# Performance work log

Measured on AMD Instinct MI355X. Metric: run time of the kernel, lower is better.

## Reference

```python
import jax, jax.numpy as jnp
import numpy as np

BN_EPS = 1e-5

def _batchnorm(x):
    # BatchNorm1d(affine=False) in training mode: per-feature batch stats, biased var
    m = jnp.mean(x, axis=0)
    v = jnp.var(x, axis=0)
    return (x - m) * jax.lax.rsqrt(v + BN_EPS)

def setup_inputs() -> dict:
    key = jax.random.key(0)
    ks = jax.random.split(key, 8)
    B, S, H, I = 2, 2048, 1024, 4096
    NE, NS, K = 16384, 128, 16
    return {
        "hidden_states": jax.random.normal(ks[0], (B, S, H), dtype=jnp.float32),
        "gate_w": jax.random.normal(ks[1], (I, H), dtype=jnp.float32) * 0.02,
        "up_w": jax.random.normal(ks[2], (I, H), dtype=jnp.float32) * 0.02,
        "down_w": jax.random.normal(ks[3], (H, I), dtype=jnp.float32) * 0.02,
        "router_x_w": jax.random.normal(ks[4], (NS, H), dtype=jnp.float32) * 0.02,
        "router_y_w": jax.random.normal(ks[5], (NS, H), dtype=jnp.float32) * 0.02,
        "up_embed": jax.random.normal(ks[6], (NE, H), dtype=jnp.float32) * 0.02,
        "down_embed": jax.random.normal(ks[7], (NE, H), dtype=jnp.float32) * 0.02,
        "top_k": K,
    }

def reference(hidden_states, gate_w, up_w, down_w, router_x_w, router_y_w, up_embed, down_embed, top_k):
    B, S, H = hidden_states.shape
    ns = router_x_w.shape[0]  # num_expert_sqrt
    x = hidden_states.reshape(-1, H)  # [N, H], N = B*S

    # product-key router: two grid log-softmaxes, outer-sum, global top-k
    lpx = jax.nn.log_softmax(_batchnorm(x @ router_x_w.T), axis=-1)  # [N, ns]
    lpy = jax.nn.log_softmax(_batchnorm(x @ router_y_w.T), axis=-1)  # [N, ns]
    all_scores = (lpx[:, :, None] + lpy[:, None, :]).reshape(-1, ns * ns)  # [N, ns^2]
    scores, indices = jax.lax.top_k(all_scores, top_k)  # [N, k]
    routing_weights = jnp.exp(scores)

    # per-token expert embedding gather + small bmm chain (PEER-style)
    ue = up_embed[indices]    # [N, k, H]
    de = down_embed[indices]  # [N, k, H]
    ew = jnp.einsum('nkh,nh->nk', ue, x)
    ew = jax.nn.silu(ew) * routing_weights
    experts_states = jnp.einsum('nk,nkh->nh', ew, de).reshape(B, S, H)

    # dense gated MLP
    dense = (jax.nn.silu(x @ gate_w.T) * (x @ up_w.T)) @ down_w.T
    return dense.reshape(B, S, H) + experts_states
```

## Files before the change

kernel.cpp:

```cpp
#include <hip/hip_runtime.h>

typedef float f32x4 __attribute__((ext_vector_type(4)));
typedef short bf16x8 __attribute__((ext_vector_type(8)));
typedef unsigned short u16;

#define NEG_INF (-1e30f)

__device__ __forceinline__ u16 f2bf(float f) {
    unsigned u = __builtin_bit_cast(unsigned, f);
    unsigned r = u + 0x7FFFu + ((u >> 16) & 1u);
    return (u16)(r >> 16);
}

__device__ __forceinline__ float wave_max(float v) {
    #pragma unroll
    for (int o = 32; o > 0; o >>= 1) v = fmaxf(v, __shfl_xor(v, o, 64));
    return v;
}
__device__ __forceinline__ float wave_sum(float v) {
    #pragma unroll
    for (int o = 32; o > 0; o >>= 1) v += __shfl_xor(v, o, 64);
    return v;
}
__device__ __forceinline__ void wave_argmax(float& v, int& i) {
    #pragma unroll
    for (int o = 32; o > 0; o >>= 1) {
        float ov = __shfl_xor(v, o, 64);
        int oi = __shfl_xor(i, o, 64);
        if (ov > v || (ov == v && oi < i)) { v = ov; i = oi; }
    }
}

__device__ __forceinline__ void g2l16(const void* g, void* l) {
    __builtin_amdgcn_global_load_lds((__attribute__((address_space(1))) void*)g,
                                     (__attribute__((address_space(3))) void*)l,
                                     16, 0, 0);
}

template<int NROUND>
__device__ __forceinline__ void stage_bf16(const u16* __restrict__ src, int ld,
                                           u16* dst, int tid) {
    #pragma unroll
    for (int r = 0; r < NROUND; ++r) {
        int e = r * 2048 + tid * 8;
        int row = e >> 6, col = e & 63;
        g2l16(src + (size_t)row * ld + col, dst + e);
    }
}

__device__ __forceinline__ void stage_f32_128(const float* __restrict__ src, int ld,
                                              u16* dst, int tid) {
    #pragma unroll
    for (int r = 0; r < 4; ++r) {
        int e = r * 2048 + tid * 8;
        int row = e >> 6, col = e & 63;
        const float* s = src + (size_t)row * ld + col;
        float4 a = *reinterpret_cast<const float4*>(s);
        float4 b = *reinterpret_cast<const float4*>(s + 4);
        uint4 pk;
        pk.x = (unsigned)f2bf(a.x) | ((unsigned)f2bf(a.y) << 16);
        pk.y = (unsigned)f2bf(a.z) | ((unsigned)f2bf(a.w) << 16);
        pk.z = (unsigned)f2bf(b.x) | ((unsigned)f2bf(b.y) << 16);
        pk.w = (unsigned)f2bf(b.z) | ((unsigned)f2bf(b.w) << 16);
        *reinterpret_cast<uint4*>(dst + e) = pk;
    }
}

__device__ __forceinline__ bf16x8 frag(const u16* lds, int row0, int ks, int lane) {
    return *reinterpret_cast<const bf16x8*>(
        lds + (row0 + (lane & 15)) * 64 + ks * 32 + (lane >> 4) * 8);
}


template<bool ABF, bool ADD>
__global__ __launch_bounds__(256, 2) void gemm_bt64(
    const float* __restrict__ Af, const u16* __restrict__ Ab, const u16* __restrict__ B,
    float* __restrict__ C, int K, int ldA, int ldB, int ldC) {
    __shared__ u16 As[8192];
    __shared__ u16 Bs[4096];
    int tid = threadIdx.x, lane = tid & 63, wave = tid >> 6;
    int rowBase = blockIdx.y * 128, colBase = blockIdx.x * 64;
    int wm = (wave >> 1) * 64, wn = (wave & 1) * 32;
    f32x4 acc[4][2] = {};
    for (int k0 = 0; k0 < K; k0 += 64) {
        if constexpr (ABF) stage_bf16<4>(Ab + (size_t)rowBase * ldA + k0, ldA, As, tid);
        else               stage_f32_128(Af + (size_t)rowBase * ldA + k0, ldA, As, tid);
        stage_bf16<2>(B + (size_t)colBase * ldB + k0, ldB, Bs, tid);
        __syncthreads();
        #pragma unroll
        for (int ks = 0; ks < 2; ++ks) {
            bf16x8 af[4], bfr[2];
            #pragma unroll
            for (int i = 0; i < 4; ++i) af[i] = frag(As, wm + i * 16, ks, lane);
            #pragma unroll
            for (int j = 0; j < 2; ++j) bfr[j] = frag(Bs, wn + j * 16, ks, lane);
            #pragma unroll
            for (int i = 0; i < 4; ++i)
                #pragma unroll
                for (int j = 0; j < 2; ++j)
                    acc[i][j] = __builtin_amdgcn_mfma_f32_16x16x32_bf16(af[i], bfr[j], acc[i][j], 0, 0, 0);
        }
        __syncthreads();
    }
    int rq = (lane >> 4) * 4, cq = lane & 15;
    #pragma unroll
    for (int i = 0; i < 4; ++i)
        #pragma unroll
        for (int j = 0; j < 2; ++j) {
            int col = colBase + wn + j * 16 + cq;
            #pragma unroll
            for (int r = 0; r < 4; ++r) {
                int row = rowBase + wm + i * 16 + rq + r;
                size_t o = (size_t)row * ldC + col;
                if constexpr (ADD) C[o] = acc[i][j][r] + C[o];
                else               C[o] = acc[i][j][r];
            }
        }
}

template<bool ABF>
__global__ __launch_bounds__(256, 2) void gemm_gateup(
    const float* __restrict__ Af, const u16* __restrict__ Ab,
    const u16* __restrict__ G, const u16* __restrict__ U,
    u16* __restrict__ H2, int ldH) {
    __shared__ u16 As[8192];
    __shared__ u16 Gs[4096];
    __shared__ u16 Us[4096];
    int tid = threadIdx.x, lane = tid & 63, wave = tid >> 6;
    int rowBase = blockIdx.y * 128, colBase = blockIdx.x * 64;
    int wm = (wave >> 1) * 64, wn = (wave & 1) * 32;
    f32x4 ag[4][2] = {}, au[4][2] = {};
    for (int k0 = 0; k0 < 1024; k0 += 64) {
        if constexpr (ABF) stage_bf16<4>(Ab + (size_t)rowBase * 1024 + k0, 1024, As, tid);
        else               stage_f32_128(Af + (size_t)rowBase * 1024 + k0, 1024, As, tid);
        stage_bf16<2>(G + (size_t)colBase * 1024 + k0, 1024, Gs, tid);
        stage_bf16<2>(U + (size_t)colBase * 1024 + k0, 1024, Us, tid);
        __syncthreads();
        #pragma unroll
        for (int ks = 0; ks < 2; ++ks) {
            bf16x8 af[4], gf[2], uf[2];
            #pragma unroll
            for (int i = 0; i < 4; ++i) af[i] = frag(As, wm + i * 16, ks, lane);
            #pragma unroll
            for (int j = 0; j < 2; ++j) { gf[j] = frag(Gs, wn + j * 16, ks, lane);
                                          uf[j] = frag(Us, wn + j * 16, ks, lane); }
            #pragma unroll
            for (int i = 0; i < 4; ++i)
                #pragma unroll
                for (int j = 0; j < 2; ++j) {
                    ag[i][j] = __builtin_amdgcn_mfma_f32_16x16x32_bf16(af[i], gf[j], ag[i][j], 0, 0, 0);
                    au[i][j] = __builtin_amdgcn_mfma_f32_16x16x32_bf16(af[i], uf[j], au[i][j], 0, 0, 0);
                }
        }
        __syncthreads();
    }
    int rq = (lane >> 4) * 4, cq = lane & 15;
    #pragma unroll
    for (int i = 0; i < 4; ++i)
        #pragma unroll
        for (int j = 0; j < 2; ++j) {
            int col = colBase + wn + j * 16 + cq;
            #pragma unroll
            for (int r = 0; r < 4; ++r) {
                int row = rowBase + wm + i * 16 + rq + r;
                float g = ag[i][j][r], u = au[i][j][r];
                float h = (g / (1.f + __expf(-g))) * u;
                H2[(size_t)row * ldH + col] = f2bf(h);
            }
        }
}

__global__ void conv_bf16(const float* __restrict__ s, u16* __restrict__ d,
                          int srcLd, int cl2, int total4) {
    int i = blockIdx.x * 256 + threadIdx.x;
    if (i >= total4) return;
    int r = i >> cl2, c = (i & ((1 << cl2) - 1)) * 4;
    float4 v = *reinterpret_cast<const float4*>(s + (size_t)r * srcLd + c);
    ushort4 pk;
    pk.x = f2bf(v.x); pk.y = f2bf(v.y); pk.z = f2bf(v.z); pk.w = f2bf(v.w);
    *reinterpret_cast<ushort4*>(d + (size_t)i * 4) = pk;
}

__global__ void bn_stats(const float* __restrict__ R, float* __restrict__ stats) {
    int c = threadIdx.x;
    int r0 = blockIdx.x * 64;
    float s = 0.f, s2 = 0.f;
    for (int r = r0; r < r0 + 64; ++r) {
        float v = R[(size_t)r * 256 + c];
        s += v; s2 += v * v;
    }
    atomicAdd(&stats[c], s);
    atomicAdd(&stats[256 + c], s2);
}

__global__ __launch_bounds__(64) void router_topk(
    const float* __restrict__ R, const float* __restrict__ stats,
    int* __restrict__ idx_out, float* __restrict__ wt_out) {
    int n = blockIdx.x, lane = threadIdx.x;
    const float invN = 1.0f / 4096.0f;
    float z[4];
    #pragma unroll
    for (int p = 0; p < 4; ++p) {
        int c = p * 64 + lane;
        float mean = stats[c] * invN;
        float var = fmaxf(stats[256 + c] * invN - mean * mean, 0.f);
        float v = R[(size_t)n * 256 + c];
        z[p] = (v - mean) * rsqrtf(var + 1e-5f);
    }
    float mx = wave_max(fmaxf(z[0], z[1]));
    float sx = __logf(wave_sum(__expf(z[0] - mx) + __expf(z[1] - mx)));
    float lx0 = z[0] - mx - sx, lx1 = z[1] - mx - sx;
    float my = wave_max(fmaxf(z[2], z[3]));
    float sy = __logf(wave_sum(__expf(z[2] - my) + __expf(z[3] - my)));
    float ly0 = z[2] - my - sy, ly1 = z[3] - my - sy;

    __shared__ float tx[16], ty[16];
    __shared__ int txc[16], tyc[16];
    float v0 = lx0, v1 = lx1;
    for (int t = 0; t < 16; ++t) {
        float bv; int bc;
        if (v1 > v0) { bv = v1; bc = lane + 64; } else { bv = v0; bc = lane; }
        wave_argmax(bv, bc);
        if (lane == 0) { tx[t] = bv; txc[t] = bc; }
        if (bc == lane) v0 = NEG_INF;
        else if (bc == lane + 64) v1 = NEG_INF;
    }
    v0 = ly0; v1 = ly1;
    for (int t = 0; t < 16; ++t) {
        float bv; int bc;
        if (v1 > v0) { bv = v1; bc = lane + 64; } else { bv = v0; bc = lane; }
        wave_argmax(bv, bc);
        if (lane == 0) { ty[t] = bv; tyc[t] = bc; }
        if (bc == lane) v0 = NEG_INF;
        else if (bc == lane + 64) v1 = NEG_INF;
    }
    __syncthreads();
    float cv[4]; int ci[4];
    #pragma unroll
    for (int p = 0; p < 4; ++p) {
        int pid = p * 64 + lane;
        cv[p] = tx[pid >> 4] + ty[pid & 15];
        ci[p] = pid;
    }
    for (int t = 0; t < 16; ++t) {
        float bv = cv[0]; int bc = ci[0];
        #pragma unroll
        for (int p = 1; p < 4; ++p)
            if (cv[p] > bv) { bv = cv[p]; bc = ci[p]; }
        wave_argmax(bv, bc);
        if (lane == 0) {
            idx_out[n * 16 + t] = txc[bc >> 4] * 128 + tyc[bc & 15];
            wt_out[n * 16 + t] = __expf(bv);
        }
        #pragma unroll
        for (int p = 0; p < 4; ++p)
            if (ci[p] == bc) cv[p] = NEG_INF;
    }
}

__global__ __launch_bounds__(256) void expert_store(
    const float* __restrict__ X, const float* __restrict__ UE, const float* __restrict__ DE,
    const int* __restrict__ idxs, const float* __restrict__ wts, float* __restrict__ Out) {
    int n = blockIdx.x, tid = threadIdx.x;
    int lane = tid & 63, wave = tid >> 6;
    __shared__ float xs[1024];
    __shared__ float ews[16];
    __shared__ int sidx[16];
    __shared__ float swt[16];
    if (tid < 16) {
        sidx[tid] = min(max(idxs[n * 16 + tid], 0), 16383);
        swt[tid] = wts[n * 16 + tid];
    }
    {
        float4 v = reinterpret_cast<const float4*>(X + (size_t)n * 1024)[tid];
        *reinterpret_cast<float4*>(xs + tid * 4) = v;
    }
    __syncthreads();
    #pragma unroll
    for (int q = 0; q < 4; ++q) {
        int e = wave * 4 + q;
        const float* row = UE + (size_t)sidx[e] * 1024;
        float acc = 0.f;
        #pragma unroll
        for (int c = 0; c < 4; ++c) {
            int h = c * 256 + lane * 4;
            float4 a = *reinterpret_cast<const float4*>(row + h);
            float4 xv = *reinterpret_cast<const float4*>(xs + h);
            acc += a.x * xv.x + a.y * xv.y + a.z * xv.z + a.w * xv.w;
        }
        acc = wave_sum(acc);
        if (lane == 0) {
            float s = acc / (1.f + __expf(-acc));
            ews[e] = s * swt[e];
        }
    }
    __syncthreads();
    float4 a = make_float4(0.f, 0.f, 0.f, 0.f);
    int h = tid * 4;
    #pragma unroll
    for (int e = 0; e < 16; ++e) {
        const float* row = DE + (size_t)sidx[e] * 1024;
        float4 v = *reinterpret_cast<const float4*>(row + h);
        float w = ews[e];
        a.x += w * v.x; a.y += w * v.y;
        a.z += w * v.z; a.w += w * v.w;
    }
    reinterpret_cast<float4*>(Out + (size_t)n * 1024)[tid] = a;
}

extern "C" void kernel_launch(void* const* d_in, const int* in_sizes, int n_in,
                              void* d_out, int out_size, void* d_ws, size_t ws_size,
                              hipStream_t stream) {
    const float* x   = (const float*)d_in[0];
    const float* gw  = (const float*)d_in[1];
    const float* uw  = (const float*)d_in[2];
    const float* dw  = (const float*)d_in[3];
    const float* rxw = (const float*)d_in[4];
    const float* ryw = (const float*)d_in[5];
    const float* ue  = (const float*)d_in[6];
    const float* de  = (const float*)d_in[7];
    float* out = (float*)d_out;

    char* p = (char*)d_ws;
    float* stats = (float*)p; p += 16384;
    int*   idxb  = (int*)p;   p += 262144;
    float* wtb   = (float*)p; p += 262144;
    u16*   W     = (u16*)p;   p += 4194304;
    float* R     = (float*)p;
    u16*   H2    = (u16*)p;

    bool useXb = ws_size >= 38289408ull + 8388608ull;
    u16* xb = (u16*)((char*)d_ws + 38289408ull);

    hipMemsetAsync(stats, 0, 512 * sizeof(float), stream);

    conv_bf16<<<128, 256, 0, stream>>>(rxw, W, 1024, 8, 32768);
    conv_bf16<<<128, 256, 0, stream>>>(ryw, W + 131072, 1024, 8, 32768);
    if (useXb) conv_bf16<<<4096, 256, 0, stream>>>(x, xb, 1024, 8, 1048576);

    if (useXb) gemm_bt64<true , false><<<dim3(4, 32), 256, 0, stream>>>(nullptr, xb, W, R, 1024, 1024, 1024, 256);
    else       gemm_bt64<false, false><<<dim3(4, 32), 256, 0, stream>>>(x, nullptr, W, R, 1024, 1024, 1024, 256);

    bn_stats<<<64, 256, 0, stream>>>(R, stats);
    router_topk<<<4096, 64, 0, stream>>>(R, stats, idxb, wtb);
    expert_store<<<4096, 256, 0, stream>>>(x, ue, de, idxb, wtb, out);

    for (int q = 0; q < 4; ++q) {
        conv_bf16<<<1024, 256, 0, stream>>>(gw + (size_t)q * 1048576, W, 1024, 8, 262144);
        conv_bf16<<<1024, 256, 0, stream>>>(uw + (size_t)q * 1048576, W + 1048576, 1024, 8, 262144);
        if (useXb) gemm_gateup<true ><<<dim3(16, 32), 256, 0, stream>>>(nullptr, xb, W, W + 1048576, H2 + q * 1024, 4096);
        else       gemm_gateup<false><<<dim3(16, 32), 256, 0, stream>>>(x, nullptr, W, W + 1048576, H2 + q * 1024, 4096);
    }
    for (int h = 0; h < 2; ++h) {
        conv_bf16<<<2048, 256, 0, stream>>>(dw + h * 2048, W, 4096, 9, 524288);
        gemm_bt64<true, true><<<dim3(16, 32), 256, 0, stream>>>(nullptr, H2 + h * 2048, W, out, 2048, 4096, 2048, 1024);
    }
}
```

Before: 547.5 us.

## Fuse fp32-to-bf16 conversion into GEMM staging and co-schedule expert with gate/up GEMM

Removes all standalone bf16 conversion passes and weight scratch buffers. GEMMs now load fp32 directly and pack to bf16 with the hardware v_cvt_pk_bf16_f32 instruction while staging LDS. The gate/up GEMM runs in one launch interleaved with the per-token expert gather blocks, and the down projection uses an XCD-aware block swizzle. This cuts launches and global traffic for converted copies, but every block that touches a weight tile re-reads and re-converts fp32 weights, and the expert path now shares a kernel whose register and LDS footprint is sized for the GEMM.

```diff
diff --git a/kernel.cpp b/kernel.cpp
--- a/kernel.cpp
+++ b/kernel.cpp
@@ -11,6 +11,11 @@
     unsigned r = u + 0x7FFFu + ((u >> 16) & 1u);
     return (u16)(r >> 16);
 }
+__device__ __forceinline__ unsigned pk2(float a, float b) {
+    unsigned r;
+    asm("v_cvt_pk_bf16_f32 %0, %1, %2" : "=v"(r) : "v"(a), "v"(b));
+    return r;
+}
 
 __device__ __forceinline__ float wave_max(float v) {
     #pragma unroll
@@ -48,20 +53,19 @@
     }
 }
 
-__device__ __forceinline__ void stage_f32_128(const float* __restrict__ src, int ld,
-                                              u16* dst, int tid) {
-    #pragma unroll
-    for (int r = 0; r < 4; ++r) {
+template<int NROUND>
+__device__ __forceinline__ void stage_f32(const float* __restrict__ src, int ld,
+                                          u16* dst, int tid) {
+    #pragma unroll
+    for (int r = 0; r < NROUND; ++r) {
         int e = r * 2048 + tid * 8;
         int row = e >> 6, col = e & 63;
         const float* s = src + (size_t)row * ld + col;
         float4 a = *reinterpret_cast<const float4*>(s);
         float4 b = *reinterpret_cast<const float4*>(s + 4);
         uint4 pk;
-        pk.x = (unsigned)f2bf(a.x) | ((unsigned)f2bf(a.y) << 16);
-        pk.y = (unsigned)f2bf(a.z) | ((unsigned)f2bf(a.w) << 16);
-        pk.z = (unsigned)f2bf(b.x) | ((unsigned)f2bf(b.y) << 16);
-        pk.w = (unsigned)f2bf(b.z) | ((unsigned)f2bf(b.w) << 16);
+        pk.x = pk2(a.x, a.y); pk.y = pk2(a.z, a.w);
+        pk.z = pk2(b.x, b.y); pk.w = pk2(b.z, b.w);
         *reinterpret_cast<uint4*>(dst + e) = pk;
     }
 }
@@ -71,21 +75,20 @@
         lds + (row0 + (lane & 15)) * 64 + ks * 32 + (lane >> 4) * 8);
 }
 
-
-template<bool ABF, bool ADD>
-__global__ __launch_bounds__(256, 2) void gemm_bt64(
-    const float* __restrict__ Af, const u16* __restrict__ Ab, const u16* __restrict__ B,
-    float* __restrict__ C, int K, int ldA, int ldB, int ldC) {
+__global__ __launch_bounds__(256, 2) void gemm_router(
+    const float* __restrict__ X, const float* __restrict__ RX, const float* __restrict__ RY,
+    float* __restrict__ R) {
     __shared__ u16 As[8192];
     __shared__ u16 Bs[4096];
     int tid = threadIdx.x, lane = tid & 63, wave = tid >> 6;
     int rowBase = blockIdx.y * 128, colBase = blockIdx.x * 64;
+    const float* Bp = (blockIdx.x < 2) ? RX + (size_t)colBase * 1024
+                                       : RY + (size_t)(colBase - 128) * 1024;
     int wm = (wave >> 1) * 64, wn = (wave & 1) * 32;
     f32x4 acc[4][2] = {};
-    for (int k0 = 0; k0 < K; k0 += 64) {
-        if constexpr (ABF) stage_bf16<4>(Ab + (size_t)rowBase * ldA + k0, ldA, As, tid);
-        else               stage_f32_128(Af + (size_t)rowBase * ldA + k0, ldA, As, tid);
-        stage_bf16<2>(B + (size_t)colBase * ldB + k0, ldB, Bs, tid);
+    for (int k0 = 0; k0 < 1024; k0 += 64) {
+        stage_f32<4>(X + (size_t)rowBase * 1024 + k0, 1024, As, tid);
+        stage_f32<2>(Bp + k0, 1024, Bs, tid);
         __syncthreads();
         #pragma unroll
         for (int ks = 0; ks < 2; ++ks) {
@@ -111,74 +114,156 @@
             #pragma unroll
             for (int r = 0; r < 4; ++r) {
                 int row = rowBase + wm + i * 16 + rq + r;
-                size_t o = (size_t)row * ldC + col;
-                if constexpr (ADD) C[o] = acc[i][j][r] + C[o];
-                else               C[o] = acc[i][j][r];
-            }
-        }
-}
-
-template<bool ABF>
-__global__ __launch_bounds__(256, 2) void gemm_gateup(
-    const float* __restrict__ Af, const u16* __restrict__ Ab,
-    const u16* __restrict__ G, const u16* __restrict__ U,
-    u16* __restrict__ H2, int ldH) {
+                R[(size_t)row * 256 + col] = acc[i][j][r];
+            }
+        }
+}
+
+__global__ __launch_bounds__(256, 2) void gateup_expert(
+    const float* __restrict__ X, const float* __restrict__ GW, const float* __restrict__ UW,
+    u16* __restrict__ H2,
+    const float* __restrict__ UE, const float* __restrict__ DE,
+    const int* __restrict__ idxs, const float* __restrict__ wts, float* __restrict__ Out) {
+    __shared__ __align__(16) char smem[32768];
+    int b = blockIdx.x, tid = threadIdx.x;
+    int lane = tid & 63, wave = tid >> 6;
+
+    if (b % 3 == 0) {
+        int g = b / 3;
+        int rowBase = (g >> 6) * 128, colBase = (g & 63) * 64;
+        u16* As = (u16*)smem;
+        u16* Gs = (u16*)(smem + 16384);
+        u16* Us = (u16*)(smem + 24576);
+        int wm = (wave >> 1) * 64, wn = (wave & 1) * 32;
+        f32x4 ag[4][2] = {}, au[4][2] = {};
+        for (int k0 = 0; k0 < 1024; k0 += 64) {
+            stage_f32<4>(X + (size_t)rowBase * 1024 + k0, 1024, As, tid);
+            stage_f32<2>(GW + (size_t)colBase * 1024 + k0, 1024, Gs, tid);
+            stage_f32<2>(UW + (size_t)colBase * 1024 + k0, 1024, Us, tid);
+            __syncthreads();
+            #pragma unroll
+            for (int ks = 0; ks < 2; ++ks) {
+                bf16x8 af[4], gf[2], uf[2];
+                #pragma unroll
+                for (int i = 0; i < 4; ++i) af[i] = frag(As, wm + i * 16, ks, lane);
+                #pragma unroll
+                for (int j = 0; j < 2; ++j) { gf[j] = frag(Gs, wn + j * 16, ks, lane);
+                                              uf[j] = frag(Us, wn + j * 16, ks, lane); }
+                #pragma unroll
+                for (int i = 0; i < 4; ++i)
+                    #pragma unroll
+                    for (int j = 0; j < 2; ++j) {
+                        ag[i][j] = __builtin_amdgcn_mfma_f32_16x16x32_bf16(af[i], gf[j], ag[i][j], 0, 0, 0);
+                        au[i][j] = __builtin_amdgcn_mfma_f32_16x16x32_bf16(af[i], uf[j], au[i][j], 0, 0, 0);
+                    }
+            }
+            __syncthreads();
+        }
+        int rq = (lane >> 4) * 4, cq = lane & 15;
+        #pragma unroll
+        for (int i = 0; i < 4; ++i)
+            #pragma unroll
+            for (int j = 0; j < 2; ++j) {
+                int col = colBase + wn + j * 16 + cq;
+                #pragma unroll
+                for (int r = 0; r < 4; ++r) {
+                    int row = rowBase + wm + i * 16 + rq + r;
+                    float gv = ag[i][j][r], uv = au[i][j][r];
+                    float h = (gv / (1.f + __expf(-gv))) * uv;
+                    H2[(size_t)row * 4096 + col] = f2bf(h);
+                }
+            }
+    } else {
+        int n = b - b / 3 - 1;
+        float* xs  = (float*)smem;
+        float* ews = (float*)(smem + 4096);
+        int*  sidx = (int*)(smem + 4160);
+        float* swt = (float*)(smem + 4224);
+        if (tid < 16) {
+            sidx[tid] = min(max(idxs[n * 16 + tid], 0), 16383);
+            swt[tid] = wts[n * 16 + tid];
+        }
+        {
+            float4 v = reinterpret_cast<const float4*>(X + (size_t)n * 1024)[tid];
+            *reinterpret_cast<float4*>(xs + tid * 4) = v;
+        }
+        __syncthreads();
+        #pragma unroll
+        for (int q = 0; q < 4; ++q) {
+            int e = wave * 4 + q;
+            const float* row = UE + (size_t)sidx[e] * 1024;
+            float acc = 0.f;
+            #pragma unroll
+            for (int c = 0; c < 4; ++c) {
+                int h = c * 256 + lane * 4;
+                float4 a = *reinterpret_cast<const float4*>(row + h);
+                float4 xv = *reinterpret_cast<const float4*>(xs + h);
+                acc += a.x * xv.x + a.y * xv.y + a.z * xv.z + a.w * xv.w;
+            }
+            acc = wave_sum(acc);
+            if (lane == 0) {
+                float s = acc / (1.f + __expf(-acc));
+                ews[e] = s * swt[e];
+            }
+        }
+        __syncthreads();
+        float4 a = make_float4(0.f, 0.f, 0.f, 0.f);
+        int h = tid * 4;
+        #pragma unroll
+        for (int e = 0; e < 16; ++e) {
+            const float* row = DE + (size_t)sidx[e] * 1024;
+            float4 v = *reinterpret_cast<const float4*>(row + h);
+            float w = ews[e];
+            a.x += w * v.x; a.y += w * v.y;
+            a.z += w * v.z; a.w += w * v.w;
+        }
+        reinterpret_cast<float4*>(Out + (size_t)n * 1024)[tid] = a;
+    }
+}
+
+__global__ __launch_bounds__(256, 2) void gemm_down_add(
+    const u16* __restrict__ H2, const float* __restrict__ DW, float* __restrict__ Out) {
     __shared__ u16 As[8192];
-    __shared__ u16 Gs[4096];
-    __shared__ u16 Us[4096];
-    int tid = threadIdx.x, lane = tid & 63, wave = tid >> 6;
-    int rowBase = blockIdx.y * 128, colBase = blockIdx.x * 64;
+    __shared__ u16 Bs[4096];
+    int b = blockIdx.x, tid = threadIdx.x;
+    int xcd = b & 7, i = b >> 3;
+    int by = xcd * 4 + (i >> 4), bx = i & 15;
+    int lane = tid & 63, wave = tid >> 6;
+    int rowBase = by * 128, colBase = bx * 64;
     int wm = (wave >> 1) * 64, wn = (wave & 1) * 32;
-    f32x4 ag[4][2] = {}, au[4][2] = {};
-    for (int k0 = 0; k0 < 1024; k0 += 64) {
-        if constexpr (ABF) stage_bf16<4>(Ab + (size_t)rowBase * 1024 + k0, 1024, As, tid);
-        else               stage_f32_128(Af + (size_t)rowBase * 1024 + k0, 1024, As, tid);
-        stage_bf16<2>(G + (size_t)colBase * 1024 + k0, 1024, Gs, tid);
-        stage_bf16<2>(U + (size_t)colBase * 1024 + k0, 1024, Us, tid);
+    f32x4 acc[4][2] = {};
+    for (int k0 = 0; k0 < 4096; k0 += 64) {
+        stage_bf16<4>(H2 + (size_t)rowBase * 4096 + k0, 4096, As, tid);
+        stage_f32<2>(DW + (size_t)colBase * 4096 + k0, 4096, Bs, tid);
         __syncthreads();
         #pragma unroll
         for (int ks = 0; ks < 2; ++ks) {
-            bf16x8 af[4], gf[2], uf[2];
-            #pragma unroll
-            for (int i = 0; i < 4; ++i) af[i] = frag(As, wm + i * 16, ks, lane);
-            #pragma unroll
-            for (int j = 0; j < 2; ++j) { gf[j] = frag(Gs, wn + j * 16, ks, lane);
-                                          uf[j] = frag(Us, wn + j * 16, ks, lane); }
-            #pragma unroll
-            for (int i = 0; i < 4; ++i)
-                #pragma unroll
-                for (int j = 0; j < 2; ++j) {
-                    ag[i][j] = __builtin_amdgcn_mfma_f32_16x16x32_bf16(af[i], gf[j], ag[i][j], 0, 0, 0);
-                    au[i][j] = __builtin_amdgcn_mfma_f32_16x16x32_bf16(af[i], uf[j], au[i][j], 0, 0, 0);
-                }
+            bf16x8 af[4], bfr[2];
+            #pragma unroll
+            for (int i2 = 0; i2 < 4; ++i2) af[i2] = frag(As, wm + i2 * 16, ks, lane);
+            #pragma unroll
+            for (int j = 0; j < 2; ++j) bfr[j] = frag(Bs, wn + j * 16, ks, lane);
+            #pragma unroll
+            for (int i2 = 0; i2 < 4; ++i2)
+                #pragma unroll
+                for (int j = 0; j < 2; ++j)
+                    acc[i2][j] = __builtin_amdgcn_mfma_f32_16x16x32_bf16(af[i2], bfr[j], acc[i2][j], 0, 0, 0);
         }
         __syncthreads();
     }
     int rq = (lane >> 4) * 4, cq = lane & 15;
     #pragma unroll
-    for (int i = 0; i < 4; ++i)
+    for (int i2 = 0; i2 < 4; ++i2)
         #pragma unroll
         for (int j = 0; j < 2; ++j) {
             int col = colBase + wn + j * 16 + cq;
             #pragma unroll
             for (int r = 0; r < 4; ++r) {
-                int row = rowBase + wm + i * 16 + rq + r;
-                float g = ag[i][j][r], u = au[i][j][r];
-                float h = (g / (1.f + __expf(-g))) * u;
-                H2[(size_t)row * ldH + col] = f2bf(h);
-            }
-        }
-}
-
-__global__ void conv_bf16(const float* __restrict__ s, u16* __restrict__ d,
-                          int srcLd, int cl2, int total4) {
-    int i = blockIdx.x * 256 + threadIdx.x;
-    if (i >= total4) return;
-    int r = i >> cl2, c = (i & ((1 << cl2) - 1)) * 4;
-    float4 v = *reinterpret_cast<const float4*>(s + (size_t)r * srcLd + c);
-    ushort4 pk;
-    pk.x = f2bf(v.x); pk.y = f2bf(v.y); pk.z = f2bf(v.z); pk.w = f2bf(v.w);
-    *reinterpret_cast<ushort4*>(d + (size_t)i * 4) = pk;
+                int row = rowBase + wm + i2 * 16 + rq + r;
+                size_t o = (size_t)row * 1024 + col;
+                Out[o] = acc[i2][j][r] + Out[o];
+            }
+        }
 }
 
 __global__ void bn_stats(const float* __restrict__ R, float* __restrict__ stats) {
@@ -256,56 +341,6 @@
         for (int p = 0; p < 4; ++p)
             if (ci[p] == bc) cv[p] = NEG_INF;
     }
-}
-
-__global__ __launch_bounds__(256) void expert_store(
-    const float* __restrict__ X, const float* __restrict__ UE, const float* __restrict__ DE,
-    const int* __restrict__ idxs, const float* __restrict__ wts, float* __restrict__ Out) {
-    int n = blockIdx.x, tid = threadIdx.x;
-    int lane = tid & 63, wave = tid >> 6;
-    __shared__ float xs[1024];
-    __shared__ float ews[16];
-    __shared__ int sidx[16];
-    __shared__ float swt[16];
-    if (tid < 16) {
-        sidx[tid] = min(max(idxs[n * 16 + tid], 0), 16383);
-        swt[tid] = wts[n * 16 + tid];
-    }
-    {
-        float4 v = reinterpret_cast<const float4*>(X + (size_t)n * 1024)[tid];
-        *reinterpret_cast<float4*>(xs + tid * 4) = v;
-    }
-    __syncthreads();
-    #pragma unroll
-    for (int q = 0; q < 4; ++q) {
-        int e = wave * 4 + q;
-        const float* row = UE + (size_t)sidx[e] * 1024;
-        float acc = 0.f;
-        #pragma unroll
-        for (int c = 0; c < 4; ++c) {
-            int h = c * 256 + lane * 4;
-            float4 a = *reinterpret_cast<const float4*>(row + h);
-            float4 xv = *reinterpret_cast<const float4*>(xs + h);
-            acc += a.x * xv.x + a.y * xv.y + a.z * xv.z + a.w * xv.w;
-        }
-        acc = wave_sum(acc);
-        if (lane == 0) {
-            float s = acc / (1.f + __expf(-acc));
-            ews[e] = s * swt[e];
-        }
-    }
-    __syncthreads();
-    float4 a = make_float4(0.f, 0.f, 0.f, 0.f);
-    int h = tid * 4;
-    #pragma unroll
-    for (int e = 0; e < 16; ++e) {
-        const float* row = DE + (size_t)sidx[e] * 1024;
-        float4 v = *reinterpret_cast<const float4*>(row + h);
-        float w = ews[e];
-        a.x += w * v.x; a.y += w * v.y;
-        a.z += w * v.z; a.w += w * v.w;
-    }
-    reinterpret_cast<float4*>(Out + (size_t)n * 1024)[tid] = a;
 }
 
 extern "C" void kernel_launch(void* const* d_in, const int* in_sizes, int n_in,
@@ -325,34 +360,13 @@
     float* stats = (float*)p; p += 16384;
     int*   idxb  = (int*)p;   p += 262144;
     float* wtb   = (float*)p; p += 262144;
-    u16*   W     = (u16*)p;   p += 4194304;
     float* R     = (float*)p;
     u16*   H2    = (u16*)p;
 
-    bool useXb = ws_size >= 38289408ull + 8388608ull;
-    u16* xb = (u16*)((char*)d_ws + 38289408ull);
-
     hipMemsetAsync(stats, 0, 512 * sizeof(float), stream);
-
-    conv_bf16<<<128, 256, 0, stream>>>(rxw, W, 1024, 8, 32768);
-    conv_bf16<<<128, 256, 0, stream>>>(ryw, W + 131072, 1024, 8, 32768);
-    if (useXb) conv_bf16<<<4096, 256, 0, stream>>>(x, xb, 1024, 8, 1048576);
-
-    if (useXb) gemm_bt64<true , false><<<dim3(4, 32), 256, 0, stream>>>(nullptr, xb, W, R, 1024, 1024, 1024, 256);
-    else       gemm_bt64<false, false><<<dim3(4, 32), 256, 0, stream>>>(x, nullptr, W, R, 1024, 1024, 1024, 256);
-
+    gemm_router<<<dim3(4, 32), 256, 0, stream>>>(x, rxw, ryw, R);
     bn_stats<<<64, 256, 0, stream>>>(R, stats);
     router_topk<<<4096, 64, 0, stream>>>(R, stats, idxb, wtb);
-    expert_store<<<4096, 256, 0, stream>>>(x, ue, de, idxb, wtb, out);
-
-    for (int q = 0; q < 4; ++q) {
-        conv_bf16<<<1024, 256, 0, stream>>>(gw + (size_t)q * 1048576, W, 1024, 8, 262144);
-        conv_bf16<<<1024, 256, 0, stream>>>(uw + (size_t)q * 1048576, W + 1048576, 1024, 8, 262144);
-        if (useXb) gemm_gateup<true ><<<dim3(16, 32), 256, 0, stream>>>(nullptr, xb, W, W + 1048576, H2 + q * 1024, 4096);
-        else       gemm_gateup<false><<<dim3(16, 32), 256, 0, stream>>>(x, nullptr, W, W + 1048576, H2 + q * 1024, 4096);
-    }
-    for (int h = 0; h < 2; ++h) {
-        conv_bf16<<<2048, 256, 0, stream>>>(dw + h * 2048, W, 4096, 9, 524288);
-        gemm_bt64<true, true><<<dim3(16, 32), 256, 0, stream>>>(nullptr, H2 + h * 2048, W, out, 2048, 4096, 2048, 1024);
-    }
-}
+    gateup_expert<<<6144, 256, 0, stream>>>(x, gw, uw, H2, ue, de, idxb, wtb, out);
+    gemm_down_add<<<512, 256, 0, stream>>>(H2, dw, out);
+}
```

New measurement: 606.8 us. 10.8% more time.
